# Kernel optimization log

Hardware: AMD Instinct MI355X
Metric: run time of the kernel (lower is better)

Reference implementation:

```python
import jax, jax.numpy as jnp
import numpy as np

HK, WK = 7, 11  # local_k


def _local_mask(H, W):
    # Equivalent to the torch buffer: 0 inside the hk x wk window centered on the
    # query position (for odd hk, wk), -inf outside. Shape (N, N), N = H*W.
    n = jnp.arange(H * W)
    hq, wq = n // W, n % W
    dh = jnp.abs(hq[:, None] - hq[None, :])
    dw = jnp.abs(wq[:, None] - wq[None, :])
    allowed = (dh <= HK // 2) & (dw <= WK // 2)
    return jnp.where(allowed, 0.0, -jnp.inf).astype(jnp.float32)


def setup_inputs() -> dict:
    key = jax.random.key(0)
    k1, k2, k3 = jax.random.split(key, 3)
    B, H, W, C = 8, 32, 64, 512
    N = H * W
    x = jax.random.normal(k1, (B, N, C), dtype=jnp.float32)
    qkv_w = jax.random.normal(k2, (3 * C, C), dtype=jnp.float32) * (C ** -0.5)
    proj_w = jax.random.normal(k3, (C, C), dtype=jnp.float32) * (C ** -0.5)
    proj_b = jnp.zeros((C,), dtype=jnp.float32)
    return {"x": x, "qkv_w": qkv_w, "proj_w": proj_w, "proj_b": proj_b, "H": H, "W": W}


def reference(x, qkv_w, proj_w, proj_b, H, W):
    B, N, C = x.shape
    num_heads = 8
    head_dim = C // num_heads
    scale = head_dim ** -0.5

    # qkv: Linear(dim, 3*dim, bias=False) -> (B, N, 3, heads, head_dim)
    qkv = (x @ qkv_w.T).reshape(B, N, 3, num_heads, head_dim)
    q = qkv[:, :, 0].transpose(0, 2, 1, 3) * scale  # (B, h, N, d)
    k = qkv[:, :, 1].transpose(0, 2, 1, 3)
    v = qkv[:, :, 2].transpose(0, 2, 1, 3)

    attn = jnp.einsum('bhnd,bhmd->bhnm', q, k)  # (B, h, N, N)
    attn = attn + _local_mask(H, W)  # broadcast over (B, h)
    attn = jax.nn.softmax(attn, axis=-1)

    out = jnp.einsum('bhnm,bhmd->bhnd', attn, v)  # (B, h, N, d)
    out = out.transpose(0, 2, 1, 3).reshape(B, N, C)
    return out @ proj_w.T + proj_b
```

## Files before the change

### kernel.cpp

```cpp
#include <hip/hip_runtime.h>
#include <hip/hip_bf16.h>

#define B_SZ 8
#define H_SZ 32
#define W_SZ 64
#define N_SZ 2048
#define C_SZ 512
#define NH 8
#define HD 64

using u16 = unsigned short;
typedef __attribute__((ext_vector_type(8))) short s16x8;
typedef __attribute__((ext_vector_type(4))) float f32x4;

__device__ __forceinline__ float bf2f(u16 u) {
    union { unsigned int i; float f; } c; c.i = ((unsigned int)u) << 16; return c.f;
}
__device__ __forceinline__ u16 f2bf(float f) {
    union { float f; unsigned int i; } c; c.f = f;
    unsigned int r = c.i + 0x7fffu + ((c.i >> 16) & 1u);
    return (u16)(r >> 16);
}

#define GLL16(gp, lp) __builtin_amdgcn_global_load_lds( \
    (const __attribute__((address_space(1))) unsigned int*)(gp), \
    (__attribute__((address_space(3))) unsigned int*)(lp), 16, 0, 0)

__device__ __forceinline__ int lds_off(int row, int chunk) {
    return (row * 8 + (chunk ^ (row & 7))) * 8;
}

#define NX4 2097152
#define NQ4 196608
#define NP4 65536
__global__ __launch_bounds__(256)
void conv_all(const float* __restrict__ x, const float* __restrict__ qw,
              const float* __restrict__ pw, u16* __restrict__ xb,
              u16* __restrict__ qwb, u16* __restrict__ pwb)
{
    const int i = blockIdx.x * 256 + threadIdx.x;
    const float* src; u16* dst; int idx; float sc = 1.0f;
    if (i < NX4)             { src = x;  dst = xb;  idx = i; }
    else if (i < NX4 + NQ4)  { src = qw; dst = qwb; idx = i - NX4;
                               if (idx < 65536) sc = 0.125f; }
    else                     { src = pw; dst = pwb; idx = i - NX4 - NQ4; }
    const float4 v = ((const float4*)src)[idx];
    ushort4 o = { f2bf(v.x * sc), f2bf(v.y * sc), f2bf(v.z * sc), f2bf(v.w * sc) };
    ((ushort4*)dst)[idx] = o;
}

template<int MODE, int NT>
__global__ __launch_bounds__(256)
void gemm_mfma(const u16* __restrict__ A, const u16* __restrict__ Bw,
               const float* __restrict__ bias,
               u16* __restrict__ q_ws, u16* __restrict__ k_ws, u16* __restrict__ v_ws,
               float* __restrict__ outp, int K)
{
    constexpr int NJ = (NT == 128) ? 4 : 2;
    __shared__ u16 As[128 * 64];
    __shared__ u16 Bs[NT * 64];
    const int t    = threadIdx.x;
    const int m0   = blockIdx.x * 128;
    const int n0   = blockIdx.y * NT;
    const int wave = t >> 6, lane = t & 63;
    const int wm   = (wave >> 1) << 6;
    const int wn   = (wave & 1) * (NJ * 16);
    const int l16  = lane & 15, quad = lane >> 4;
    const int srow = t >> 3;
    const int sch  = (t & 7) ^ (srow & 7);

    f32x4 acc[4][NJ] = {};

    for (int k0 = 0; k0 < K; k0 += 64) {
        __syncthreads();
        #pragma unroll
        for (int g = 0; g < 4; ++g)
            GLL16(A + (size_t)(m0 + 32 * g + srow) * K + k0 + sch * 8,
                  &As[g * 2048 + t * 8]);
        #pragma unroll
        for (int g = 0; g < NT / 32; ++g)
            GLL16(Bw + (size_t)(n0 + 32 * g + srow) * K + k0 + sch * 8,
                  &Bs[g * 2048 + t * 8]);
        __syncthreads();

        s16x8 af[4][2], bf[NJ][2];
        #pragma unroll
        for (int i = 0; i < 4; ++i) {
            const int R = wm + 16 * i + l16;
            af[i][0] = *(const s16x8*)&As[lds_off(R, quad)];
            af[i][1] = *(const s16x8*)&As[lds_off(R, 4 + quad)];
        }
        #pragma unroll
        for (int j = 0; j < NJ; ++j) {
            const int R = wn + 16 * j + l16;
            bf[j][0] = *(const s16x8*)&Bs[lds_off(R, quad)];
            bf[j][1] = *(const s16x8*)&Bs[lds_off(R, 4 + quad)];
        }
        #pragma unroll
        for (int i = 0; i < 4; ++i)
            #pragma unroll
            for (int j = 0; j < NJ; ++j) {
                acc[i][j] = __builtin_amdgcn_mfma_f32_16x16x32_bf16(af[i][0], bf[j][0], acc[i][j], 0, 0, 0);
                acc[i][j] = __builtin_amdgcn_mfma_f32_16x16x32_bf16(af[i][1], bf[j][1], acc[i][j], 0, 0, 0);
            }
    }

    if (MODE == 0) {
        const int bb  = m0 >> 11;
        const int nnb = (m0 & 2047) + wm + (quad << 2);
        if (n0 >= 1024) {
            #pragma unroll
            for (int j = 0; j < NJ; ++j) {
                const int c  = n0 - 1024 + wn + 16 * j + l16;
                const int h  = c >> 6, dd = c & 63;
                u16* vp = v_ws + (((size_t)bb * NH + h) * HD + dd) * N_SZ + nnb;
                #pragma unroll
                for (int i = 0; i < 4; ++i) {
                    ushort4 st = { f2bf(acc[i][j][0]), f2bf(acc[i][j][1]),
                                   f2bf(acc[i][j][2]), f2bf(acc[i][j][3]) };
                    *(ushort4*)(vp + 16 * i) = st;
                }
            }
        } else {
            u16* T = (n0 < 512) ? q_ws : k_ws;
            #pragma unroll
            for (int j = 0; j < NJ; ++j) {
                const int gn = n0 + wn + 16 * j + l16;
                const int h  = (gn >> 6) & 7, dd = gn & 63;
                u16* tp = T + (((size_t)bb * NH + h) * N_SZ + nnb) * HD + dd;
                #pragma unroll
                for (int i = 0; i < 4; ++i)
                    #pragma unroll
                    for (int r = 0; r < 4; ++r)
                        tp[(size_t)(16 * i + r) * HD] = f2bf(acc[i][j][r]);
            }
        }
    } else {
        #pragma unroll
        for (int j = 0; j < NJ; ++j) {
            const int gn = n0 + wn + 16 * j + l16;
            const float bv = bias[gn];
            #pragma unroll
            for (int i = 0; i < 4; ++i)
                #pragma unroll
                for (int r = 0; r < 4; ++r)
                    outp[(size_t)(m0 + wm + 16 * i + (quad << 2) + r) * C_SZ + gn]
                        = acc[i][j][r] + bv;
        }
    }
}

__global__ __launch_bounds__(256)
void attn_mfma(const u16* __restrict__ q_ws, const u16* __restrict__ k_ws,
               const u16* __restrict__ vt_ws, u16* __restrict__ o_ws)
{
    __shared__ u16 KV[2][64 * 64];
    __shared__ u16 Ps[4][16 * 40];

    const int t = threadIdx.x, wave = t >> 6, lane = t & 63;
    const int l16 = lane & 15, quad = lane >> 4;
    const int u  = blockIdx.x;
    const int p  = u & 15;
    const int bh = u >> 4;
    const int r0 = 2 * p, r1 = 2 * p + 1;
    const size_t base = (size_t)bh * (N_SZ * HD);
    const int srow = t >> 3;
    const int sch  = (t & 7) ^ (srow & 7);

    const u16* qg = q_ws + base + (size_t)r0 * (64 * HD);
    u16* Qst = &KV[0][0];
    #pragma unroll
    for (int g = 0; g < 4; ++g)
        GLL16(qg + (size_t)(srow + 32 * g) * 64 + sch * 8, Qst + g * 2048 + t * 8);
    __syncthreads();

    s16x8 aQ[2][2];
    #pragma unroll
    for (int s = 0; s < 2; ++s) {
        const int Rq = 64 * s + 16 * wave + l16;
        aQ[s][0] = *(const s16x8*)&Qst[lds_off(Rq, quad)];
        aQ[s][1] = *(const s16x8*)&Qst[lds_off(Rq, 4 + quad)];
    }

    const int kb = min(max(16 * wave - 8, 0), 32);

    f32x4 accO[2][4] = {};
    float lp[2][4] = {};

    const int hlo = (r0 - 3 < 0) ? 0 : r0 - 3;
    const int hhi = (r1 + 3 > H_SZ - 1) ? H_SZ - 1 : r1 + 3;

    for (int hh = hlo; hh <= hhi; ++hh) {
        __syncthreads();
        const u16* kg = k_ws + base + (size_t)hh * (64 * HD);
        GLL16(kg + (size_t)srow        * 64 + sch * 8, &KV[0][t * 8]);
        GLL16(kg + (size_t)(srow + 32) * 64 + sch * 8, &KV[0][2048 + t * 8]);
        const u16* vg = vt_ws + base + (size_t)hh * 64;
        GLL16(vg + (size_t)srow        * N_SZ + sch * 8, &KV[1][t * 8]);
        GLL16(vg + (size_t)(srow + 32) * N_SZ + sch * 8, &KV[1][2048 + t * 8]);
        __syncthreads();

        s16x8 bK[2][2];
        #pragma unroll
        for (int j = 0; j < 2; ++j) {
            const int Rk = kb + 16 * j + l16;
            bK[j][0] = *(const s16x8*)&KV[0][lds_off(Rk, quad)];
            bK[j][1] = *(const s16x8*)&KV[0][lds_off(Rk, 4 + quad)];
        }
        s16x8 vf[4];
        #pragma unroll
        for (int j = 0; j < 4; ++j)
            vf[j] = *(const s16x8*)&KV[1][lds_off(16 * j + l16, (kb >> 3) + quad)];

        #pragma unroll
        for (int s = 0; s < 2; ++s) {
            const int dh = hh - (r0 + s);
            if (dh * dh > 9) continue;
            f32x4 z[2] = {{0.f,0.f,0.f,0.f},{0.f,0.f,0.f,0.f}};
            #pragma unroll
            for (int j = 0; j < 2; ++j) {
                z[j] = __builtin_amdgcn_mfma_f32_16x16x32_bf16(aQ[s][0], bK[j][0], z[j], 0, 0, 0);
                z[j] = __builtin_amdgcn_mfma_f32_16x16x32_bf16(aQ[s][1], bK[j][1], z[j], 0, 0, 0);
            }
            #pragma unroll
            for (int j = 0; j < 2; ++j) {
                const int ww = kb + 16 * j + l16;
                #pragma unroll
                for (int r = 0; r < 4; ++r) {
                    const int dw = ww - (16 * wave + quad * 4 + r);
                    const float pv = (dw * dw <= 25) ? __expf(z[j][r]) : 0.f;
                    const u16 pb = f2bf(pv);
                    lp[s][r] += bf2f(pb);
                    Ps[wave][(quad * 4 + r) * 40 + 16 * j + l16] = pb;
                }
            }
            s16x8 aP = *(const s16x8*)&Ps[wave][l16 * 40 + quad * 8];
            #pragma unroll
            for (int j = 0; j < 4; ++j)
                accO[s][j] = __builtin_amdgcn_mfma_f32_16x16x32_bf16(aP, vf[j], accO[s][j], 0, 0, 0);
        }
    }

    #pragma unroll
    for (int s = 0; s < 2; ++s)
        #pragma unroll
        for (int r = 0; r < 4; ++r) {
            lp[s][r] += __shfl_xor(lp[s][r], 1);
            lp[s][r] += __shfl_xor(lp[s][r], 2);
            lp[s][r] += __shfl_xor(lp[s][r], 4);
            lp[s][r] += __shfl_xor(lp[s][r], 8);
        }

    const int bb = bh >> 3, h = bh & 7;
    #pragma unroll
    for (int s = 0; s < 2; ++s)
        #pragma unroll
        for (int j = 0; j < 4; ++j)
            #pragma unroll
            for (int r = 0; r < 4; ++r) {
                const int row = (r0 + s) * 64 + 16 * wave + quad * 4 + r;
                o_ws[((size_t)bb * N_SZ + row) * C_SZ + h * 64 + 16 * j + l16]
                    = f2bf(accO[s][j][r] / lp[s][r]);
            }
}

extern "C" void kernel_launch(void* const* d_in, const int* in_sizes, int n_in,
                              void* d_out, int out_size, void* d_ws, size_t ws_size,
                              hipStream_t stream)
{
    const float* x      = (const float*)d_in[0];
    const float* qkv_w  = (const float*)d_in[1];
    const float* proj_w = (const float*)d_in[2];
    const float* proj_b = (const float*)d_in[3];
    float* outp = (float*)d_out;

    const size_t seg = (size_t)B_SZ * NH * N_SZ * HD;
    u16* q_ws = (u16*)d_ws;
    u16* k_ws = q_ws + seg;
    u16* v_ws = k_ws + seg;
    u16* o_ws = v_ws + seg;
    u16* xb   = o_ws + seg;
    u16* qwb  = xb + (size_t)16384 * 512;
    u16* pwb  = qwb + (size_t)1536 * 512;

    conv_all<<<9216, 256, 0, stream>>>(x, qkv_w, proj_w, xb, qwb, pwb);

    gemm_mfma<0, 128><<<dim3(128, 12), 256, 0, stream>>>(xb, qwb, nullptr,
                                                         q_ws, k_ws, v_ws, nullptr, C_SZ);
    attn_mfma<<<B_SZ * NH * (H_SZ / 2), 256, 0, stream>>>(q_ws, k_ws, v_ws, o_ws);
    gemm_mfma<1, 64><<<dim3(128, 8), 256, 0, stream>>>(o_ws, pwb, proj_b,
                                                       nullptr, nullptr, nullptr, outp, C_SZ);
}
```

Measured before the change: 171.5 us.

## Rewrite GEMMs with 256x128 tiles, double-buffered LDS prefetch and XCD-aware block remap

Replaces both projection GEMMs with a 512-thread kernel using 256x128 output tiles. The kernel double-buffers the A/B tiles in LDS and prefetches the next K-slice with global_load_lds while the current slice is multiplied, using explicit vmcnt waits. It also remaps block IDs across XCDs and raises wave priority during the MFMA section. This aims to hide global-load latency and improve operand reuse, at the cost of more LDS (96KB per block) and fewer blocks for the small projection GEMM (256 blocks).

```diff
diff --git a/kernel.cpp b/kernel.cpp
--- a/kernel.cpp
+++ b/kernel.cpp
@@ -49,60 +49,83 @@
     ((ushort4*)dst)[idx] = o;
 }
 
-template<int MODE, int NT>
-__global__ __launch_bounds__(256)
-void gemm_mfma(const u16* __restrict__ A, const u16* __restrict__ Bw,
-               const float* __restrict__ bias,
-               u16* __restrict__ q_ws, u16* __restrict__ k_ws, u16* __restrict__ v_ws,
-               float* __restrict__ outp, int K)
+template<int MODE, int NB>
+__global__ __launch_bounds__(512, 2)
+void gemm2(const u16* __restrict__ A, const u16* __restrict__ Bw,
+           const float* __restrict__ bias,
+           u16* __restrict__ q_ws, u16* __restrict__ k_ws, u16* __restrict__ v_ws,
+           float* __restrict__ outp)
 {
-    constexpr int NJ = (NT == 128) ? 4 : 2;
-    __shared__ u16 As[128 * 64];
-    __shared__ u16 Bs[NT * 64];
-    const int t    = threadIdx.x;
-    const int m0   = blockIdx.x * 128;
-    const int n0   = blockIdx.y * NT;
+    __shared__ u16 As[2][256 * 64];
+    __shared__ u16 Bs[2][128 * 64];
+    const int t = threadIdx.x;
+    const int chunk = gridDim.x >> 3;
+    const int wg = (blockIdx.x & 7) * chunk + (blockIdx.x >> 3);
+    const int m0 = (wg / NB) * 256;
+    const int n0 = (wg % NB) * 128;
     const int wave = t >> 6, lane = t & 63;
-    const int wm   = (wave >> 1) << 6;
-    const int wn   = (wave & 1) * (NJ * 16);
-    const int l16  = lane & 15, quad = lane >> 4;
+    const int wm = (wave >> 1) * 64;
+    const int wn = (wave & 1) * 64;
+    const int l16 = lane & 15, quad = lane >> 4;
     const int srow = t >> 3;
     const int sch  = (t & 7) ^ (srow & 7);
 
-    f32x4 acc[4][NJ] = {};
-
-    for (int k0 = 0; k0 < K; k0 += 64) {
-        __syncthreads();
-        #pragma unroll
-        for (int g = 0; g < 4; ++g)
-            GLL16(A + (size_t)(m0 + 32 * g + srow) * K + k0 + sch * 8,
-                  &As[g * 2048 + t * 8]);
-        #pragma unroll
-        for (int g = 0; g < NT / 32; ++g)
-            GLL16(Bw + (size_t)(n0 + 32 * g + srow) * K + k0 + sch * 8,
-                  &Bs[g * 2048 + t * 8]);
-        __syncthreads();
-
-        s16x8 af[4][2], bf[NJ][2];
+    const u16* Ab = A  + (size_t)(m0 + srow) * C_SZ + sch * 8;
+    const u16* Bb = Bw + (size_t)(n0 + srow) * C_SZ + sch * 8;
+
+    f32x4 acc[4][4] = {};
+
+    #pragma unroll
+    for (int g = 0; g < 4; ++g)
+        GLL16(Ab + (size_t)(64 * g) * C_SZ, &As[0][g * 4096 + t * 8]);
+    #pragma unroll
+    for (int g = 0; g < 2; ++g)
+        GLL16(Bb + (size_t)(64 * g) * C_SZ, &Bs[0][g * 4096 + t * 8]);
+
+    #pragma unroll
+    for (int tt = 0; tt < 8; ++tt) {
+        const int cur = tt & 1;
+        if (tt < 7) {
+            const int k0 = (tt + 1) * 64;
+            #pragma unroll
+            for (int g = 0; g < 4; ++g)
+                GLL16(Ab + (size_t)(64 * g) * C_SZ + k0, &As[cur ^ 1][g * 4096 + t * 8]);
+            #pragma unroll
+            for (int g = 0; g < 2; ++g)
+                GLL16(Bb + (size_t)(64 * g) * C_SZ + k0, &Bs[cur ^ 1][g * 4096 + t * 8]);
+            asm volatile("s_waitcnt vmcnt(6)" ::: "memory");
+        } else {
+            asm volatile("s_waitcnt vmcnt(0)" ::: "memory");
+        }
+        __builtin_amdgcn_s_barrier();
+        __builtin_amdgcn_sched_barrier(0);
+
+        s16x8 af[4][2], bf[4][2];
         #pragma unroll
         for (int i = 0; i < 4; ++i) {
             const int R = wm + 16 * i + l16;
-            af[i][0] = *(const s16x8*)&As[lds_off(R, quad)];
-            af[i][1] = *(const s16x8*)&As[lds_off(R, 4 + quad)];
-        }
-        #pragma unroll
-        for (int j = 0; j < NJ; ++j) {
+            af[i][0] = *(const s16x8*)&As[cur][lds_off(R, quad)];
+            af[i][1] = *(const s16x8*)&As[cur][lds_off(R, 4 + quad)];
+        }
+        #pragma unroll
+        for (int j = 0; j < 4; ++j) {
             const int R = wn + 16 * j + l16;
-            bf[j][0] = *(const s16x8*)&Bs[lds_off(R, quad)];
-            bf[j][1] = *(const s16x8*)&Bs[lds_off(R, 4 + quad)];
-        }
+            bf[j][0] = *(const s16x8*)&Bs[cur][lds_off(R, quad)];
+            bf[j][1] = *(const s16x8*)&Bs[cur][lds_off(R, 4 + quad)];
+        }
+        asm volatile("s_waitcnt lgkmcnt(0)" ::: "memory");
+        __builtin_amdgcn_s_barrier();
+        __builtin_amdgcn_sched_barrier(0);
+
+        __builtin_amdgcn_s_setprio(1);
         #pragma unroll
         for (int i = 0; i < 4; ++i)
             #pragma unroll
-            for (int j = 0; j < NJ; ++j) {
+            for (int j = 0; j < 4; ++j) {
                 acc[i][j] = __builtin_amdgcn_mfma_f32_16x16x32_bf16(af[i][0], bf[j][0], acc[i][j], 0, 0, 0);
                 acc[i][j] = __builtin_amdgcn_mfma_f32_16x16x32_bf16(af[i][1], bf[j][1], acc[i][j], 0, 0, 0);
             }
+        __builtin_amdgcn_s_setprio(0);
     }
 
     if (MODE == 0) {
@@ -110,7 +133,7 @@
         const int nnb = (m0 & 2047) + wm + (quad << 2);
         if (n0 >= 1024) {
             #pragma unroll
-            for (int j = 0; j < NJ; ++j) {
+            for (int j = 0; j < 4; ++j) {
                 const int c  = n0 - 1024 + wn + 16 * j + l16;
                 const int h  = c >> 6, dd = c & 63;
                 u16* vp = v_ws + (((size_t)bb * NH + h) * HD + dd) * N_SZ + nnb;
@@ -123,10 +146,11 @@
             }
         } else {
             u16* T = (n0 < 512) ? q_ws : k_ws;
-            #pragma unroll
-            for (int j = 0; j < NJ; ++j) {
-                const int gn = n0 + wn + 16 * j + l16;
-                const int h  = (gn >> 6) & 7, dd = gn & 63;
+            const int nq = n0 & 511;
+            #pragma unroll
+            for (int j = 0; j < 4; ++j) {
+                const int gn = nq + wn + 16 * j + l16;
+                const int h  = gn >> 6, dd = gn & 63;
                 u16* tp = T + (((size_t)bb * NH + h) * N_SZ + nnb) * HD + dd;
                 #pragma unroll
                 for (int i = 0; i < 4; ++i)
@@ -137,7 +161,7 @@
         }
     } else {
         #pragma unroll
-        for (int j = 0; j < NJ; ++j) {
+        for (int j = 0; j < 4; ++j) {
             const int gn = n0 + wn + 16 * j + l16;
             const float bv = bias[gn];
             #pragma unroll
@@ -285,9 +309,9 @@
 
     conv_all<<<9216, 256, 0, stream>>>(x, qkv_w, proj_w, xb, qwb, pwb);
 
-    gemm_mfma<0, 128><<<dim3(128, 12), 256, 0, stream>>>(xb, qwb, nullptr,
-                                                         q_ws, k_ws, v_ws, nullptr, C_SZ);
+    gemm2<0, 12><<<768, 512, 0, stream>>>(xb, qwb, nullptr,
+                                          q_ws, k_ws, v_ws, nullptr);
     attn_mfma<<<B_SZ * NH * (H_SZ / 2), 256, 0, stream>>>(q_ws, k_ws, v_ws, o_ws);
-    gemm_mfma<1, 64><<<dim3(128, 8), 256, 0, stream>>>(o_ws, pwb, proj_b,
-                                                       nullptr, nullptr, nullptr, outp, C_SZ);
-}
+    gemm2<1, 4><<<256, 512, 0, stream>>>(o_ws, pwb, proj_b,
+                                         nullptr, nullptr, nullptr, outp);
+}
```

Result: no change. 174.0 us (+1.5%).
